# Optimization experiments

Hardware: AMD Instinct MI355X
Metric: run time of the kernel (lower is better)

## Reference

```python
import jax, jax.numpy as jnp
import numpy as np

B, N, E, H = 4, 1024, 1024, 16
D = E // H

def setup_inputs() -> dict:
    key = jax.random.key(0)
    ks = jax.random.split(key, 5)
    return {
        "x": jax.random.normal(ks[0], (B, N, E), dtype=jnp.float32),
        "Wqkv": jax.random.normal(ks[1], (E, 3 * E), dtype=jnp.float32) * 0.02,
        "bqkv": jax.random.normal(ks[2], (3 * E,), dtype=jnp.float32) * 0.02,
        "Wfc": jax.random.normal(ks[3], (E, E), dtype=jnp.float32) * 0.02,
        "bfc": jax.random.normal(ks[4], (E,), dtype=jnp.float32) * 0.02,
    }

def reference(x, Wqkv, bqkv, Wfc, bfc):
    b, n, e = x.shape
    h, d = H, E // H
    qkv = x @ Wqkv + bqkv                      # [b, n, 3e]
    q, k, v = jnp.split(qkv, 3, axis=-1)       # each [b, n, e]
    # view to [b, n, h, d] then RAW reshape to [b, h, n, d] (faithful to original,
    # which uses .reshape, not transpose — mixes seq/head axes)
    q = q.reshape(b, n, h, d).reshape(b, h, n, d)
    k = k.reshape(b, n, h, d).reshape(b, h, n, d)
    v = v.reshape(b, n, h, d).reshape(b, h, n, d)
    scores = jnp.einsum('bhqd,bhkd->bhqk', q, k) / jnp.sqrt(jnp.float32(d))
    causal = jnp.triu(jnp.ones((n, n), dtype=bool), k=1)  # True above diagonal
    scores = jnp.where(causal, -jnp.inf, scores)
    attn = jax.nn.softmax(scores, axis=-1)
    out = jnp.einsum('bhqk,bhkd->bhqd', attn, v)          # [b, h, n, d]
    # raw reshape back to [b, n, h, d] then flatten heads (faithful)
    out = out.reshape(b, n, h, d).reshape(b, n, e)
    return out @ Wfc + bfc
```

## Files before the change

### kernel.cpp

```cpp
#include <hip/hip_runtime.h>


typedef __bf16 bf16x8 __attribute__((ext_vector_type(8)));
typedef float f32x4 __attribute__((ext_vector_type(4)));

#define QSCALE 0.18033688011112042f
#define DEFER_THR 11.0f

__device__ __forceinline__ unsigned short f2bf(float f) {
    unsigned u = __float_as_uint(f);
    u += 0x7fffu + ((u >> 16) & 1u);
    return (unsigned short)(u >> 16);
}

__device__ __forceinline__ unsigned cvtpk_bf16(float lo, float hi) {
    unsigned r;
    asm("v_cvt_pk_bf16_f32 %0, %1, %2" : "=v"(r) : "v"(lo), "v"(hi));
    return r;
}

union FragU { uint4 u; bf16x8 v; };

__device__ __forceinline__ bf16x8 ld_frag(const unsigned short* p) {
    FragU x; x.u = *(const uint4*)p; return x.v;
}

__device__ __forceinline__ void gload_lds16(const void* g, void* l) {
    __builtin_amdgcn_global_load_lds(
        (const __attribute__((address_space(1))) void*)g,
        (__attribute__((address_space(3))) void*)l, 16, 0, 0);
}

__global__ void cvt_bf16(const float* __restrict__ in, unsigned short* __restrict__ out, int n4) {
    int i = blockIdx.x * blockDim.x + threadIdx.x;
    int stride = gridDim.x * blockDim.x;
    for (; i < n4; i += stride) {
        float4 f = ((const float4*)in)[i];
        unsigned a = (unsigned)f2bf(f.x) | ((unsigned)f2bf(f.y) << 16);
        unsigned b = (unsigned)f2bf(f.z) | ((unsigned)f2bf(f.w) << 16);
        ((uint2*)out)[i] = make_uint2(a, b);
    }
}

__global__ void transpose_cvt(const float* __restrict__ W, unsigned short* __restrict__ Wt,
                              int rows, int cols) {
    __shared__ float tile[32][33];
    int c0 = blockIdx.x * 32, r0 = blockIdx.y * 32;
    for (int i = threadIdx.y; i < 32; i += 8)
        tile[i][threadIdx.x] = W[(r0 + i) * cols + c0 + threadIdx.x];
    __syncthreads();
    for (int i = threadIdx.y; i < 32; i += 8)
        Wt[(c0 + i) * (long)rows + r0 + threadIdx.x] = f2bf(tile[threadIdx.x][i]);
}

__global__ void transpose_v(const unsigned short* __restrict__ v,
                            unsigned short* __restrict__ vt) {
    __shared__ unsigned short tile[32][33];
    int bh = blockIdx.z;
    int n0 = blockIdx.x * 32, d0 = blockIdx.y * 32;
    const unsigned short* src = v + (long)bh * 65536;
    unsigned short* dst = vt + (long)bh * 65536;
    for (int i = threadIdx.y; i < 32; i += 8)
        tile[i][threadIdx.x] = src[(n0 + i) * 64 + d0 + threadIdx.x];
    __syncthreads();
    for (int i = threadIdx.y; i < 32; i += 8)
        dst[(d0 + i) * 1024 + n0 + threadIdx.x] = tile[threadIdx.x][i];
}

template <int MODE>
__global__ __launch_bounds__(256) void gemm128(
    const unsigned short* __restrict__ A,
    const unsigned short* __restrict__ Bt,
    const float* __restrict__ bias,
    unsigned short* __restrict__ qb,
    unsigned short* __restrict__ kb,
    unsigned short* __restrict__ vb,
    float* __restrict__ outf)
{
    const int K = 1024;
    __shared__ unsigned short As[2][4096];
    __shared__ unsigned short Bs[2][4096];
    int t = threadIdx.x, lane = t & 63, w = t >> 6;
    int wm = w >> 1, wn = w & 1;
    int lrow = lane >> 4, lcol = lane & 15;
    int tn0 = blockIdx.x * 128, tm0 = blockIdx.y * 128;

    int seg0 = w * 1024;
    int seg1 = (w + 4) * 1024;
    int off0 = seg0 + lane * 16, off1 = seg1 + lane * 16;
    int r0 = off0 >> 6, cb0 = off0 & 63;
    int r1 = off1 >> 6, cb1 = off1 & 63;

    const char* gA = (const char*)A;
    const char* gB = (const char*)Bt;

    f32x4 acc[4][4] = {};

    auto STAGE = [&](int buf, int kt) {
        long kby = (long)kt * 2;
        gload_lds16(gA + (long)(tm0 + r0) * 2048 + kby + cb0, (char*)&As[buf][0] + seg0);
        gload_lds16(gA + (long)(tm0 + r1) * 2048 + kby + cb1, (char*)&As[buf][0] + seg1);
        gload_lds16(gB + (long)(tn0 + r0) * 2048 + kby + cb0, (char*)&Bs[buf][0] + seg0);
        gload_lds16(gB + (long)(tn0 + r1) * 2048 + kby + cb1, (char*)&Bs[buf][0] + seg1);
    };

    STAGE(0, 0);
    asm volatile("s_waitcnt vmcnt(0)");
    __syncthreads();

    int cur = 0;
    for (int kt = 0; kt < K; kt += 32) {
        if (kt + 32 < K) STAGE(cur ^ 1, kt + 32);

        bf16x8 af[4], bfr[4];
        #pragma unroll
        for (int mi = 0; mi < 4; ++mi)
            af[mi] = ld_frag(&As[cur][0] + (wm * 64 + mi * 16 + lcol) * 32 + lrow * 8);
        #pragma unroll
        for (int ni = 0; ni < 4; ++ni)
            bfr[ni] = ld_frag(&Bs[cur][0] + (wn * 64 + ni * 16 + lcol) * 32 + lrow * 8);
        #pragma unroll
        for (int mi = 0; mi < 4; ++mi)
            #pragma unroll
            for (int ni = 0; ni < 4; ++ni)
                acc[mi][ni] = __builtin_amdgcn_mfma_f32_16x16x32_bf16(af[mi], bfr[ni], acc[mi][ni], 0, 0, 0);

        __syncthreads();
        cur ^= 1;
    }

    #pragma unroll
    for (int mi = 0; mi < 4; ++mi) {
        int gr0 = tm0 + wm * 64 + mi * 16 + lrow * 4;
        #pragma unroll
        for (int ni = 0; ni < 4; ++ni) {
            int gc = tn0 + wn * 64 + ni * 16 + lcol;
            float bv = bias[gc];
            if (MODE == 0) {
                int sec = gc >> 10, ei = gc & 1023;
                unsigned short* dst = sec == 0 ? qb : (sec == 1 ? kb : vb);
                if (sec == 0) {
                    #pragma unroll
                    for (int r = 0; r < 4; ++r)
                        dst[(long)(gr0 + r) * 1024 + ei] = f2bf((acc[mi][ni][r] + bv) * QSCALE);
                } else {
                    #pragma unroll
                    for (int r = 0; r < 4; ++r)
                        dst[(long)(gr0 + r) * 1024 + ei] = f2bf(acc[mi][ni][r] + bv);
                }
            } else {
                #pragma unroll
                for (int r = 0; r < 4; ++r)
                    outf[(long)(gr0 + r) * 1024 + gc] = acc[mi][ni][r] + bv;
            }
        }
    }
}

__global__ __launch_bounds__(256) void attn(
    const unsigned short* __restrict__ qbuf,
    const unsigned short* __restrict__ kbuf,
    const unsigned short* __restrict__ vtbuf,
    unsigned short* __restrict__ obuf)
{
    __shared__ char smem[4 * 32 * 68 * 4 + 512 + 512] __attribute__((aligned(16)));
    unsigned short (*Ps)[32][40] = (unsigned short (*)[32][40])smem;
    float* accS = (float*)smem;
    float* mS = (float*)(smem + 4 * 32 * 68 * 4);
    float* lS = mS + 128;

    int id = blockIdx.x;
    int xcd = id & 7, slot = id >> 3;
    int bh = xcd + 8 * (slot >> 4);
    int j = slot & 15;

    const unsigned short* Q  = qbuf + (long)bh * 65536;
    const unsigned short* Kp = kbuf + (long)bh * 65536;
    const unsigned short* VT = vtbuf + (long)bh * 65536;
    unsigned short* O = obuf + (long)bh * 65536;
    int t = threadIdx.x, lane = t & 63, w = t >> 6;
    int lrow = lane >> 4, lcol = lane & 15;
    const float NEG = -__builtin_inff();

    #pragma unroll
    for (int pass = 0; pass < 2; ++pass) {
        int qt = pass == 0 ? j : 31 - j;
        int qbase = qt * 32;
        int T = qt + 1;

        bf16x8 qf[2][2];
        #pragma unroll
        for (int qg = 0; qg < 2; ++qg)
            #pragma unroll
            for (int kc = 0; kc < 2; ++kc)
                qf[qg][kc] = ld_frag(Q + (long)(qbase + qg * 16 + lcol) * 64 + kc * 32 + lrow * 8);

        f32x4 acc[2][4] = {};
        float m_i[2] = {NEG, NEG}, l_i[2] = {0.f, 0.f};

        if (w < T) {
            int kt = w * 32;
            bf16x8 kf[2][2];
            #pragma unroll
            for (int kg = 0; kg < 2; ++kg)
                #pragma unroll
                for (int kc = 0; kc < 2; ++kc)
                    kf[kg][kc] = ld_frag(Kp + (long)(kt + kg * 16 + lcol) * 64 + kc * 32 + lrow * 8);

            for (;; kt += 128) {
                f32x4 s[2][2] = {};
                __builtin_amdgcn_s_setprio(1);
                #pragma unroll
                for (int kg = 0; kg < 2; ++kg)
                    #pragma unroll
                    for (int kc = 0; kc < 2; ++kc) {
                        s[0][kg] = __builtin_amdgcn_mfma_f32_16x16x32_bf16(kf[kg][kc], qf[0][kc], s[0][kg], 0, 0, 0);
                        s[1][kg] = __builtin_amdgcn_mfma_f32_16x16x32_bf16(kf[kg][kc], qf[1][kc], s[1][kg], 0, 0, 0);
                    }
                __builtin_amdgcn_s_setprio(0);

                bool more = kt + 128 < T * 32;
                bf16x8 kn[2][2];
                if (more) {
                    #pragma unroll
                    for (int kg = 0; kg < 2; ++kg)
                        #pragma unroll
                        for (int kc = 0; kc < 2; ++kc)
                            kn[kg][kc] = ld_frag(Kp + (long)(kt + 128 + kg * 16 + lcol) * 64 + kc * 32 + lrow * 8);
                }
                bf16x8 vf[4];
                #pragma unroll
                for (int dg = 0; dg < 4; ++dg)
                    vf[dg] = ld_frag(VT + (long)(dg * 16 + lcol) * 1024 + kt + lrow * 8);

                float tv[2][8], lmax[2];
                bool diag = (kt == qbase);
                #pragma unroll
                for (int qg = 0; qg < 2; ++qg) {
                    #pragma unroll
                    for (int kg = 0; kg < 2; ++kg)
                        #pragma unroll
                        for (int r = 0; r < 4; ++r)
                            tv[qg][kg * 4 + r] = s[qg][kg][r];
                    if (diag) {
                        #pragma unroll
                        for (int kg = 0; kg < 2; ++kg)
                            #pragma unroll
                            for (int r = 0; r < 4; ++r)
                                if (kg * 16 + lrow * 4 + r > qg * 16 + lcol)
                                    tv[qg][kg * 4 + r] = NEG;
                    }
                    float a0 = fmaxf(tv[qg][0], tv[qg][1]), a1 = fmaxf(tv[qg][2], tv[qg][3]);
                    float a2 = fmaxf(tv[qg][4], tv[qg][5]), a3 = fmaxf(tv[qg][6], tv[qg][7]);
                    lmax[qg] = fmaxf(fmaxf(a0, a1), fmaxf(a2, a3));
                }

                bool ok = (lmax[0] <= m_i[0] + DEFER_THR) && (lmax[1] <= m_i[1] + DEFER_THR);
                if (!__all(ok)) {
                    #pragma unroll
                    for (int qg = 0; qg < 2; ++qg) {
                        float mx = fmaxf(lmax[qg], __shfl_xor(lmax[qg], 16));
                        mx = fmaxf(mx, __shfl_xor(mx, 32));
                        float mnew = fmaxf(m_i[qg], mx);
                        float alpha = exp2f(m_i[qg] - mnew);
                        m_i[qg] = mnew;
                        l_i[qg] *= alpha;
                        #pragma unroll
                        for (int dg = 0; dg < 4; ++dg)
                            #pragma unroll
                            for (int r = 0; r < 4; ++r)
                                acc[qg][dg][r] *= alpha;
                    }
                }

                #pragma unroll
                for (int qg = 0; qg < 2; ++qg) {
                    float p[8], ps = 0.f;
                    #pragma unroll
                    for (int jj = 0; jj < 8; ++jj) { p[jj] = exp2f(tv[qg][jj] - m_i[qg]); ps += p[jj]; }
                    unsigned u0 = cvtpk_bf16(p[0], p[1]);
                    unsigned u1 = cvtpk_bf16(p[2], p[3]);
                    unsigned u2 = cvtpk_bf16(p[4], p[5]);
                    unsigned u3 = cvtpk_bf16(p[6], p[7]);
                    *(uint2*)&Ps[w][qg * 16 + lcol][lrow * 4]      = make_uint2(u0, u1);
                    *(uint2*)&Ps[w][qg * 16 + lcol][16 + lrow * 4] = make_uint2(u2, u3);
                    ps += __shfl_xor(ps, 16);
                    ps += __shfl_xor(ps, 32);
                    l_i[qg] += ps;
                }

                bf16x8 pb[2];
                pb[0] = ld_frag(&Ps[w][lcol][lrow * 8]);
                pb[1] = ld_frag(&Ps[w][16 + lcol][lrow * 8]);
                __builtin_amdgcn_s_setprio(1);
                #pragma unroll
                for (int dg = 0; dg < 4; ++dg) {
                    acc[0][dg] = __builtin_amdgcn_mfma_f32_16x16x32_bf16(vf[dg], pb[0], acc[0][dg], 0, 0, 0);
                    acc[1][dg] = __builtin_amdgcn_mfma_f32_16x16x32_bf16(vf[dg], pb[1], acc[1][dg], 0, 0, 0);
                }
                __builtin_amdgcn_s_setprio(0);

                if (!more) break;
                #pragma unroll
                for (int kg = 0; kg < 2; ++kg)
                    #pragma unroll
                    for (int kc = 0; kc < 2; ++kc)
                        kf[kg][kc] = kn[kg][kc];
            }
        }

        __syncthreads();
        #pragma unroll
        for (int qg = 0; qg < 2; ++qg) {
            int q = qg * 16 + lcol;
            if (lrow == 0) { mS[w * 32 + q] = m_i[qg]; lS[w * 32 + q] = l_i[qg]; }
            #pragma unroll
            for (int dg = 0; dg < 4; ++dg)
                *(f32x4*)&accS[(w * 32 + q) * 68 + dg * 16 + lrow * 4] = acc[qg][dg];
        }
        __syncthreads();

        {
            int qq = t >> 3, d0 = (t & 7) * 8;
            float m0 = mS[qq], m1 = mS[32 + qq], m2 = mS[64 + qq], m3 = mS[96 + qq];
            float M = fmaxf(fmaxf(m0, m1), fmaxf(m2, m3));
            float e0 = exp2f(m0 - M), e1 = exp2f(m1 - M), e2 = exp2f(m2 - M), e3 = exp2f(m3 - M);
            float L = e0 * lS[qq] + e1 * lS[32 + qq] + e2 * lS[64 + qq] + e3 * lS[96 + qq];
            float inv = 1.f / L;
            const float* a0 = &accS[qq * 68 + d0];
            const float* a1 = &accS[(32 + qq) * 68 + d0];
            const float* a2 = &accS[(64 + qq) * 68 + d0];
            const float* a3 = &accS[(96 + qq) * 68 + d0];
            unsigned short h[8];
            #pragma unroll
            for (int jj = 0; jj < 8; ++jj)
                h[jj] = f2bf((e0 * a0[jj] + e1 * a1[jj] + e2 * a2[jj] + e3 * a3[jj]) * inv);
            uint4 pk;
            pk.x = (unsigned)h[0] | ((unsigned)h[1] << 16);
            pk.y = (unsigned)h[2] | ((unsigned)h[3] << 16);
            pk.z = (unsigned)h[4] | ((unsigned)h[5] << 16);
            pk.w = (unsigned)h[6] | ((unsigned)h[7] << 16);
            *(uint4*)&O[(long)(qbase + qq) * 64 + d0] = pk;
        }
        __syncthreads();
    }
}

extern "C" void kernel_launch(void* const* d_in, const int* in_sizes, int n_in,
                              void* d_out, int out_size, void* d_ws, size_t ws_size,
                              hipStream_t stream) {
    const float* x    = (const float*)d_in[0];
    const float* Wqkv = (const float*)d_in[1];
    const float* bqkv = (const float*)d_in[2];
    const float* Wfc  = (const float*)d_in[3];
    const float* bfc  = (const float*)d_in[4];
    float* out = (float*)d_out;

    unsigned short* ws    = (unsigned short*)d_ws;
    unsigned short* xb    = ws;
    unsigned short* wqkvT = xb + (4u << 20);
    unsigned short* wfcT  = wqkvT + (3u << 20);
    unsigned short* qb    = wfcT + (1u << 20);
    unsigned short* kb    = qb + (4u << 20);
    unsigned short* vb    = kb + (4u << 20);
    unsigned short* vbT   = xb;
    unsigned short* ob    = vb;

    cvt_bf16<<<dim3(2048), dim3(256), 0, stream>>>(x, xb, (4 << 20) / 4);
    transpose_cvt<<<dim3(3072 / 32, 1024 / 32), dim3(32, 8), 0, stream>>>(Wqkv, wqkvT, 1024, 3072);
    transpose_cvt<<<dim3(1024 / 32, 1024 / 32), dim3(32, 8), 0, stream>>>(Wfc, wfcT, 1024, 1024);

    gemm128<0><<<dim3(24, 32), dim3(256), 0, stream>>>(xb, wqkvT, bqkv, qb, kb, vb, nullptr);
    transpose_v<<<dim3(32, 2, 64), dim3(32, 8), 0, stream>>>(vb, vbT);
    attn<<<dim3(1024), dim3(256), 0, stream>>>(qb, kb, vbT, ob);
    gemm128<1><<<dim3(8, 32), dim3(256), 0, stream>>>(ob, wfcT, bfc, nullptr, nullptr, nullptr, out);
}
```

Measured before the change: 123.4 us.

## Shrink attention LDS and registers: fp16 partials, deferred row-sum reduction, occupancy hint

The cross-wave merge now stores normalized partial outputs in fp16 and folds the row sum into a log-sum-exp max, which roughly halves the shared-memory footprint. Per-iteration cross-lane shuffles for the softmax denominator are replaced by per-lane partial sums that are reduced once at the end. The next K fragments now load directly into the live registers, removing the copy, and launch_bounds requests 6 blocks per unit. The aim is higher occupancy and fewer shuffles per tile, at the cost of fp16 precision in the partial outputs and possible register spills if the occupancy target is too tight.

Measured after the change: 210.9 us. 1.71x slower.

```diff
diff --git a/kernel.cpp b/kernel.cpp
--- a/kernel.cpp
+++ b/kernel.cpp
@@ -157,17 +157,16 @@
     }
 }
 
-__global__ __launch_bounds__(256) void attn(
+__global__ __launch_bounds__(256, 6) void attn(
     const unsigned short* __restrict__ qbuf,
     const unsigned short* __restrict__ kbuf,
     const unsigned short* __restrict__ vtbuf,
     unsigned short* __restrict__ obuf)
 {
-    __shared__ char smem[4 * 32 * 68 * 4 + 512 + 512] __attribute__((aligned(16)));
+    __shared__ char smem[17920] __attribute__((aligned(16)));
     unsigned short (*Ps)[32][40] = (unsigned short (*)[32][40])smem;
-    float* accS = (float*)smem;
-    float* mS = (float*)(smem + 4 * 32 * 68 * 4);
-    float* lS = mS + 128;
+    _Float16* accH = (_Float16*)smem;
+    float* mS = (float*)(smem + 17408);
 
     int id = blockIdx.x;
     int xcd = id & 7, slot = id >> 3;
@@ -196,7 +195,8 @@
                 qf[qg][kc] = ld_frag(Q + (long)(qbase + qg * 16 + lcol) * 64 + kc * 32 + lrow * 8);
 
         f32x4 acc[2][4] = {};
-        float m_i[2] = {NEG, NEG}, l_i[2] = {0.f, 0.f};
+        float m_i[2] = {NEG, NEG};
+        float lsum[2][2] = {{0.f, 0.f}, {0.f, 0.f}};
 
         if (w < T) {
             int kt = w * 32;
@@ -207,7 +207,7 @@
                 for (int kc = 0; kc < 2; ++kc)
                     kf[kg][kc] = ld_frag(Kp + (long)(kt + kg * 16 + lcol) * 64 + kc * 32 + lrow * 8);
 
-            for (;; kt += 128) {
+            for (;;) {
                 f32x4 s[2][2] = {};
                 __builtin_amdgcn_s_setprio(1);
                 #pragma unroll
@@ -219,14 +219,14 @@
                     }
                 __builtin_amdgcn_s_setprio(0);
 
-                bool more = kt + 128 < T * 32;
-                bf16x8 kn[2][2];
+                int ktn = kt + 128;
+                bool more = ktn < T * 32;
                 if (more) {
                     #pragma unroll
                     for (int kg = 0; kg < 2; ++kg)
                         #pragma unroll
                         for (int kc = 0; kc < 2; ++kc)
-                            kn[kg][kc] = ld_frag(Kp + (long)(kt + 128 + kg * 16 + lcol) * 64 + kc * 32 + lrow * 8);
+                            kf[kg][kc] = ld_frag(Kp + (long)(ktn + kg * 16 + lcol) * 64 + kc * 32 + lrow * 8);
                 }
                 bf16x8 vf[4];
                 #pragma unroll
@@ -264,7 +264,8 @@
                         float mnew = fmaxf(m_i[qg], mx);
                         float alpha = exp2f(m_i[qg] - mnew);
                         m_i[qg] = mnew;
-                        l_i[qg] *= alpha;
+                        lsum[qg][0] *= alpha;
+                        lsum[qg][1] *= alpha;
                         #pragma unroll
                         for (int dg = 0; dg < 4; ++dg)
                             #pragma unroll
@@ -275,18 +276,17 @@
 
                 #pragma unroll
                 for (int qg = 0; qg < 2; ++qg) {
-                    float p[8], ps = 0.f;
-                    #pragma unroll
-                    for (int jj = 0; jj < 8; ++jj) { p[jj] = exp2f(tv[qg][jj] - m_i[qg]); ps += p[jj]; }
+                    float p[8];
+                    #pragma unroll
+                    for (int jj = 0; jj < 8; ++jj) p[jj] = exp2f(tv[qg][jj] - m_i[qg]);
+                    lsum[qg][0] += (p[0] + p[1]) + (p[2] + p[3]);
+                    lsum[qg][1] += (p[4] + p[5]) + (p[6] + p[7]);
                     unsigned u0 = cvtpk_bf16(p[0], p[1]);
                     unsigned u1 = cvtpk_bf16(p[2], p[3]);
                     unsigned u2 = cvtpk_bf16(p[4], p[5]);
                     unsigned u3 = cvtpk_bf16(p[6], p[7]);
                     *(uint2*)&Ps[w][qg * 16 + lcol][lrow * 4]      = make_uint2(u0, u1);
                     *(uint2*)&Ps[w][qg * 16 + lcol][16 + lrow * 4] = make_uint2(u2, u3);
-                    ps += __shfl_xor(ps, 16);
-                    ps += __shfl_xor(ps, 32);
-                    l_i[qg] += ps;
                 }
 
                 bf16x8 pb[2];
@@ -301,11 +301,7 @@
                 __builtin_amdgcn_s_setprio(0);
 
                 if (!more) break;
-                #pragma unroll
-                for (int kg = 0; kg < 2; ++kg)
-                    #pragma unroll
-                    for (int kc = 0; kc < 2; ++kc)
-                        kf[kg][kc] = kn[kg][kc];
+                kt = ktn;
             }
         }
 
@@ -313,10 +309,22 @@
         #pragma unroll
         for (int qg = 0; qg < 2; ++qg) {
             int q = qg * 16 + lcol;
-            if (lrow == 0) { mS[w * 32 + q] = m_i[qg]; lS[w * 32 + q] = l_i[qg]; }
-            #pragma unroll
-            for (int dg = 0; dg < 4; ++dg)
-                *(f32x4*)&accS[(w * 32 + q) * 68 + dg * 16 + lrow * 4] = acc[qg][dg];
+            float lr = lsum[qg][0] + lsum[qg][1];
+            lr += __shfl_xor(lr, 16);
+            lr += __shfl_xor(lr, 32);
+            float mprime, inv;
+            if (lr > 0.f) { mprime = m_i[qg] + log2f(lr); inv = 1.f / lr; }
+            else          { mprime = NEG; inv = 0.f; }
+            if (lrow == 0) mS[w * 32 + q] = mprime;
+            #pragma unroll
+            for (int dg = 0; dg < 4; ++dg) {
+                _Float16 a0 = (_Float16)(acc[qg][dg][0] * inv);
+                _Float16 a1 = (_Float16)(acc[qg][dg][1] * inv);
+                _Float16 a2 = (_Float16)(acc[qg][dg][2] * inv);
+                _Float16 a3 = (_Float16)(acc[qg][dg][3] * inv);
+                _Float16* dst = &accH[(w * 32 + q) * 68 + dg * 16 + lrow * 4];
+                dst[0] = a0; dst[1] = a1; dst[2] = a2; dst[3] = a3;
+            }
         }
         __syncthreads();
 
@@ -325,16 +333,16 @@
             float m0 = mS[qq], m1 = mS[32 + qq], m2 = mS[64 + qq], m3 = mS[96 + qq];
             float M = fmaxf(fmaxf(m0, m1), fmaxf(m2, m3));
             float e0 = exp2f(m0 - M), e1 = exp2f(m1 - M), e2 = exp2f(m2 - M), e3 = exp2f(m3 - M);
-            float L = e0 * lS[qq] + e1 * lS[32 + qq] + e2 * lS[64 + qq] + e3 * lS[96 + qq];
-            float inv = 1.f / L;
-            const float* a0 = &accS[qq * 68 + d0];
-            const float* a1 = &accS[(32 + qq) * 68 + d0];
-            const float* a2 = &accS[(64 + qq) * 68 + d0];
-            const float* a3 = &accS[(96 + qq) * 68 + d0];
+            float inv = 1.f / (e0 + e1 + e2 + e3);
+            const _Float16* a0 = &accH[qq * 68 + d0];
+            const _Float16* a1 = &accH[(32 + qq) * 68 + d0];
+            const _Float16* a2 = &accH[(64 + qq) * 68 + d0];
+            const _Float16* a3 = &accH[(96 + qq) * 68 + d0];
             unsigned short h[8];
             #pragma unroll
             for (int jj = 0; jj < 8; ++jj)
-                h[jj] = f2bf((e0 * a0[jj] + e1 * a1[jj] + e2 * a2[jj] + e3 * a3[jj]) * inv);
+                h[jj] = f2bf((e0 * (float)a0[jj] + e1 * (float)a1[jj] +
+                              e2 * (float)a2[jj] + e3 * (float)a3[jj]) * inv);
             uint4 pk;
             pk.x = (unsigned)h[0] | ((unsigned)h[1] << 16);
             pk.y = (unsigned)h[2] | ((unsigned)h[3] << 16);
```
